# Kernel tuning notes

Measured on AMD Instinct MI355X. Metric: run time of the kernel, lower is better.

Reference implementation:

```python
import jax, jax.numpy as jnp
import numpy as np

H = 512          # hidden_size
SH = 120         # scoring_net_hidden_size
B = 1024         # batch
S = 64           # num_sentences


def setup_inputs() -> dict:
    key = jax.random.key(0)
    ks = jax.random.split(key, 12)
    sc = 0.05
    return {
        "C": jax.random.normal(ks[0], (B, S, H), jnp.float32),
        "Q": jax.random.normal(ks[1], (B, 1, H), jnp.float32),
        "prev_M": jax.random.normal(ks[2], (B, 1, H), jnp.float32),
        # scoring network params: fc1: 4H -> SH, fc2: SH -> 1
        "fc1_w": jax.random.normal(ks[3], (SH, 4 * H), jnp.float32) * sc,
        "fc1_b": jnp.zeros((SH,), jnp.float32),
        "fc2_w": jax.random.normal(ks[4], (1, SH), jnp.float32) * sc,
        "fc2_b": jnp.zeros((1,), jnp.float32),
        # GRU params (torch layout: rows ordered r, z, n)
        "W_ih": jax.random.normal(ks[5], (3 * H, H), jnp.float32) * sc,
        "W_hh": jax.random.normal(ks[6], (3 * H, H), jnp.float32) * sc,
        "b_ih": jnp.zeros((3 * H,), jnp.float32),
        "b_hh": jnp.zeros((3 * H,), jnp.float32),
    }


def reference(C, Q, prev_M, fc1_w, fc1_b, fc2_w, fc2_b, W_ih, W_hh, b_ih, b_hh):
    # --- scoring network (arch=1 feature vector) ---
    feat = jnp.concatenate(
        [C * Q, C * prev_M, jnp.abs(C - Q), jnp.abs(C - prev_M)], axis=2
    )  # [B, S, 4H]
    h1 = jnp.tanh(jnp.einsum("bsf,kf->bsk", feat, fc1_w) + fc1_b)
    G = jax.nn.sigmoid((jnp.einsum("bsk,ok->bso", h1, fc2_w) + fc2_b)[..., 0])  # [B, S]

    # --- gated GRU memory update over sentences ---
    xg_all = jnp.einsum("bsh,gh->bsg", C, W_ih) + b_ih  # [B, S, 3H] precomputed input gates

    def step(h, inp):
        xg, g = inp  # xg: [B, 3H], g: [B]
        hg = h @ W_hh.T + b_hh
        xr, xz, xn = jnp.split(xg, 3, axis=-1)
        hr, hz, hn = jnp.split(hg, 3, axis=-1)
        r = jax.nn.sigmoid(xr + hr)
        z = jax.nn.sigmoid(xz + hz)
        n = jnp.tanh(xn + r * hn)
        h_gru = (1.0 - z) * n + z * h          # standard torch GRU update
        g = g[:, None]
        h_new = g * h_gru + (1.0 - g) * h      # episodic gating
        return h_new, None

    h0 = jnp.zeros((C.shape[0], H), C.dtype)
    h_final, _ = jax.lax.scan(step, h0, (xg_all.transpose(1, 0, 2), G.T))
    return h_final[:, None, :]  # [B, 1, H]
```

## Files before the change

kernel.cpp:

```cpp
#include <hip/hip_runtime.h>
#include <hip/hip_bf16.h>

#define H_ 512
#define SH_ 120
#define B_ 1024
#define S_ 64

typedef __bf16 bf16x8 __attribute__((ext_vector_type(8)));
typedef float floatx4 __attribute__((ext_vector_type(4)));

__device__ __forceinline__ float bf2f(ushort u) {
    union { unsigned int i; float f; } v; v.i = ((unsigned int)u) << 16; return v.f;
}
__device__ __forceinline__ ushort f2bf(float f) {
    union { float f; unsigned int i; } v; v.f = f;
    unsigned int x = v.i;
    unsigned int r = (x + 0x7fffu + ((x >> 16) & 1u)) >> 16;
    return (ushort)r;
}

__device__ __attribute__((aligned(64))) unsigned g_prog[256];

__global__ __launch_bounds__(256) void prep_w(
    const float* __restrict__ fc1w, ushort* __restrict__ fc1wb,
    const float* __restrict__ Wih,  ushort* __restrict__ Wihb,
    const float* __restrict__ Whh,  ushort* __restrict__ Whhb)
{
    const int stride = gridDim.x * blockDim.x;
    const int tid = blockIdx.x * blockDim.x + threadIdx.x;
    for (int i = tid; i < 61440; i += stride) {
        const float4 v = ((const float4*)fc1w)[i];
        ushort4 o; o.x = f2bf(v.x); o.y = f2bf(v.y); o.z = f2bf(v.z); o.w = f2bf(v.w);
        ((ushort4*)fc1wb)[i] = o;
    }
    for (int i = tid; i < 196608; i += stride) {
        const float4 v = ((const float4*)Wih)[i];
        ushort4 o; o.x = f2bf(v.x); o.y = f2bf(v.y); o.z = f2bf(v.z); o.w = f2bf(v.w);
        ((ushort4*)Wihb)[i] = o;
    }
    for (int i = tid; i < 196608; i += stride) {
        const float4 v = ((const float4*)Whh)[i];
        ushort4 o; o.x = f2bf(v.x); o.y = f2bf(v.y); o.z = f2bf(v.z); o.w = f2bf(v.w);
        ((ushort4*)Whhb)[i] = o;
    }
}

__global__ __launch_bounds__(256) void g_kernel(
    const float* __restrict__ C, const float* __restrict__ Q,
    const float* __restrict__ M, const ushort* __restrict__ fc1wb,
    const float* __restrict__ fc1b, const float* __restrict__ fc2w,
    const float* __restrict__ fc2b, float* __restrict__ G)
{
    __shared__ float qrow[H_];
    __shared__ float mrow[H_];
    __shared__ __align__(16) ushort featT[64 * 72];
    __shared__ __align__(16) ushort wT[128 * 72];
    __shared__ float h1s[64 * 132];

    const int b = blockIdx.x;
    const int t = threadIdx.x;
    for (int i = t; i < H_; i += 256) { qrow[i] = Q[(size_t)b * H_ + i]; mrow[i] = M[(size_t)b * H_ + i]; }

    const int wrow = t >> 1;
    const int wc0  = (t & 1) * 32;
    if (wrow >= SH_) {
        uint4* dst = (uint4*)&wT[wrow * 72 + wc0];
        const uint4 z = {0u, 0u, 0u, 0u};
        dst[0] = z; dst[1] = z; dst[2] = z; dst[3] = z;
    }
    __syncthreads();

    const int lane = t & 63;
    const int wv   = t >> 6;
    const int quad = lane >> 4;
    const int l15  = lane & 15;
    const int arow = wv * 16 + l15;
    const int s    = t >> 2;
    const int c0   = (t & 3) * 16;

    floatx4 acc[8];
#pragma unroll
    for (int i = 0; i < 8; ++i) acc[i] = (floatx4){0.f, 0.f, 0.f, 0.f};

    for (int hc = 0; hc < H_; hc += 64) {
        float cr[16];
        {
            const float4* csrc = (const float4*)(C + ((size_t)b * S_ + s) * H_ + hc + c0);
            *(float4*)&cr[0]  = csrc[0];
            *(float4*)&cr[4]  = csrc[1];
            *(float4*)&cr[8]  = csrc[2];
            *(float4*)&cr[12] = csrc[3];
        }
#pragma unroll
        for (int seg = 0; seg < 4; ++seg) {
#pragma unroll
            for (int u = 0; u < 16; ++u) {
                const int kk = c0 + u;
                const float c = cr[u];
                const float o = (seg == 0 || seg == 2) ? qrow[hc + kk] : mrow[hc + kk];
                const float v = (seg < 2) ? c * o : fabsf(c - o);
                featT[s * 72 + kk] = f2bf(v);
            }
            if (wrow < SH_) {
                const uint4* src = (const uint4*)(fc1wb + (size_t)wrow * (4 * H_) + seg * H_ + hc + wc0);
                uint4* dst = (uint4*)&wT[wrow * 72 + wc0];
                dst[0] = src[0]; dst[1] = src[1]; dst[2] = src[2]; dst[3] = src[3];
            }
            __syncthreads();
#pragma unroll
            for (int ks = 0; ks < 64; ks += 32) {
                const int ao = ks + quad * 8;
                const bf16x8 af = *(const bf16x8*)&featT[arow * 72 + ao];
#pragma unroll
                for (int nt = 0; nt < 8; ++nt) {
                    const bf16x8 bfr = *(const bf16x8*)&wT[(nt * 16 + l15) * 72 + ao];
                    acc[nt] = __builtin_amdgcn_mfma_f32_16x16x32_bf16(af, bfr, acc[nt], 0, 0, 0);
                }
            }
            __syncthreads();
        }
    }

#pragma unroll
    for (int nt = 0; nt < 8; ++nt) {
        const int col = nt * 16 + l15;
        const float bias = (col < SH_) ? fc1b[col] : 0.f;
#pragma unroll
        for (int r = 0; r < 4; ++r) {
            const int row = wv * 16 + quad * 4 + r;
            h1s[row * 132 + col] = (col < SH_) ? tanhf(acc[nt][r] + bias) : 0.f;
        }
    }
    __syncthreads();
    {
        const int part = t & 3;
        float sum = 0.f;
        for (int k = part; k < SH_; k += 4) sum += h1s[s * 132 + k] * fc2w[k];
        sum += __shfl_xor(sum, 1);
        sum += __shfl_xor(sum, 2);
        if (part == 0) {
            const float logit = sum + fc2b[0];
            G[(size_t)b * S_ + s] = 1.f / (1.f + expf(-logit));
        }
    }
}

__global__ __launch_bounds__(256) void scan_all(
    const float* __restrict__ C, const ushort* __restrict__ Wihb,
    const ushort* __restrict__ Whhb, const float* __restrict__ bih,
    const float* __restrict__ bhh, const float* __restrict__ G,
    uint* __restrict__ hp0, uint* __restrict__ hp1,
    float* __restrict__ out)
{
    __shared__ __align__(16) ushort Whh_s[96 * 520];
    __shared__ __align__(16) char  smem_u[55296];
    ushort* AsU = (ushort*)smem_u;
    float*  gs  = (float*)smem_u;

    const int bx = blockIdx.x;
    const int jt = bx >> 4;
    const int bt = ((bx & 7) << 1) | ((bx >> 3) & 1);
    const int jb = jt * 32;
    const int bb = bt * 64;
    const int t  = threadIdx.x;
    const int lane = t & 63;
    const int wv   = t >> 6;
    const int quad = lane >> 4;
    const int l15  = lane & 15;
    const int mh   = wv >> 1;
    const int cset = wv & 1;
    const int crow = t >> 2;
    const int cc0  = (t & 3) * 16;
    const int hrow = t >> 2;
    const int hseg = t & 3;

    const unsigned vbase = __hip_atomic_load(&g_prog[(bt << 4) + jt],
                                             __ATOMIC_RELAXED, __HIP_MEMORY_SCOPE_AGENT);

#pragma unroll
    for (int i = 0; i < 24; ++i) {
        const int gid = i * 256 + t;
        const int row = gid >> 6;
        const int grp = gid & 63;
        const int grow = (row >> 5) * H_ + jb + (row & 31);
        *(uint4*)&Whh_s[row * 520 + grp * 8] =
            *(const uint4*)(Whhb + (size_t)grow * H_ + grp * 8);
    }

    float br_[2], bz_[2], bxn_[2], bhn_[2];
#pragma unroll
    for (int nt = 0; nt < 2; ++nt) {
        const int j = jb + nt * 16 + l15;
        br_[nt]  = bih[j] + bhh[j];
        bz_[nt]  = bih[H_ + j] + bhh[H_ + j];
        bxn_[nt] = bih[2 * H_ + j];
        bhn_[nt] = bhh[2 * H_ + j];
    }

    const int hold_kc  = (jb >> 6) << 6;
    const int hold_off = jb & 63;

    const uint* hr = hp0;
    uint*       hw = hp1;

    float cr[16];
    unsigned long long hreg[8];
    bf16x8 bi[3][2];

    auto load_c = [&](int tstep, int kc) {
        const float4* src = (const float4*)(C + ((size_t)(bb + crow) * S_ + tstep) * H_ + kc + cc0);
        *(float4*)&cr[0]  = src[0];
        *(float4*)&cr[4]  = src[1];
        *(float4*)&cr[8]  = src[2];
        *(float4*)&cr[12] = src[3];
    };
    auto load_h = [&](int kc) {
        const unsigned long long* src = (const unsigned long long*)
            (hr + (size_t)(bb + hrow) * H_ + kc + hseg * 16);
#pragma unroll
        for (int i = 0; i < 8; ++i)
            hreg[i] = __hip_atomic_load(src + i, __ATOMIC_RELAXED, __HIP_MEMORY_SCOPE_AGENT);
    };
    auto loadBi = [&](int kc) {
#pragma unroll
        for (int ct = 0; ct < 3; ++ct) {
            const int ctg = cset * 3 + ct;
            const size_t wrow = (size_t)((ctg >> 1) * H_ + jb + (ctg & 1) * 16 + l15) * H_;
#pragma unroll
            for (int ks2 = 0; ks2 < 2; ++ks2)
                bi[ct][ks2] = *(const bf16x8*)(Wihb + wrow + kc + ks2 * 32 + quad * 8);
        }
    };
    auto write_As = [&](int buf) {
        ushort* base = AsU + buf * 13824;
        __align__(16) ushort cb[16];
#pragma unroll
        for (int u = 0; u < 16; ++u) cb[u] = f2bf(cr[u]);
        uint4* d = (uint4*)&base[crow * 72 + cc0];
        d[0] = ((uint4*)cb)[0]; d[1] = ((uint4*)cb)[1];
        uint hiu[8], lou[8];
#pragma unroll
        for (int i = 0; i < 8; ++i) {
            const uint p0 = (uint)(hreg[i] & 0xFFFFFFFFull);
            const uint p1 = (uint)(hreg[i] >> 32);
            hiu[i] = (p0 >> 16) | (p1 & 0xFFFF0000u);
            lou[i] = (p0 & 0xFFFFu) | (p1 << 16);
        }
        uint4* dh = (uint4*)&base[4608 + hrow * 72 + hseg * 16];
        dh[0] = *(uint4*)&hiu[0]; dh[1] = *(uint4*)&hiu[4];
        uint4* dl = (uint4*)&base[9216 + hrow * 72 + hseg * 16];
        dl[0] = *(uint4*)&lou[0]; dl[1] = *(uint4*)&lou[4];
    };

    load_c(0, 0); loadBi(0); load_h(0);
    write_As(0);
    __syncthreads();

    for (int tstep = 0; tstep < S_; ++tstep) {
        float g_[4];
#pragma unroll
        for (int r4 = 0; r4 < 4; ++r4)
            g_[r4] = G[(size_t)(bb + wv * 16 + quad * 4 + r4) * S_ + tstep];

        floatx4 accA[2][3], accB[2][2];
#pragma unroll
        for (int rf = 0; rf < 2; ++rf) {
#pragma unroll
            for (int i = 0; i < 3; ++i) accA[rf][i] = (floatx4){0.f, 0.f, 0.f, 0.f};
#pragma unroll
            for (int i = 0; i < 2; ++i) accB[rf][i] = (floatx4){0.f, 0.f, 0.f, 0.f};
        }
        float hold_[2][4];

        for (int kc = 0; kc < H_; kc += 64) {
            const int cur = (kc >> 6) & 1;
            const int kn  = kc + 64;
            if (kn < H_) { load_c(tstep, kn); load_h(kn); }
            const ushort* Ac = AsU + cur * 13824;
            const ushort* Ah = Ac + 4608;
            const ushort* Al = Ac + 9216;
#pragma unroll
            for (int ks2 = 0; ks2 < 2; ++ks2) {
                const int ao = ks2 * 32 + quad * 8;
                bf16x8 a_c[2], a_hh[2], a_hl[2];
#pragma unroll
                for (int rf = 0; rf < 2; ++rf) {
                    const int ai = (mh * 32 + rf * 16 + l15) * 72 + ao;
                    a_c[rf]  = *(const bf16x8*)&Ac[ai];
                    a_hh[rf] = *(const bf16x8*)&Ah[ai];
                    a_hl[rf] = *(const bf16x8*)&Al[ai];
                }
#pragma unroll
                for (int ct = 0; ct < 3; ++ct) {
                    const int ctg = cset * 3 + ct;
                    const bf16x8 bh = *(const bf16x8*)
                        &Whh_s[((ctg >> 1) * 32 + (ctg & 1) * 16 + l15) * 520 + kc + ao];
#pragma unroll
                    for (int rf = 0; rf < 2; ++rf) {
                        if (ct >= 1 && cset == 1) {
                            accA[rf][ct]     = __builtin_amdgcn_mfma_f32_16x16x32_bf16(a_c[rf],  bi[ct][ks2], accA[rf][ct],     0, 0, 0);
                            accB[rf][ct - 1] = __builtin_amdgcn_mfma_f32_16x16x32_bf16(a_hh[rf], bh,          accB[rf][ct - 1], 0, 0, 0);
                            accB[rf][ct - 1] = __builtin_amdgcn_mfma_f32_16x16x32_bf16(a_hl[rf], bh,          accB[rf][ct - 1], 0, 0, 0);
                        } else {
                            accA[rf][ct] = __builtin_amdgcn_mfma_f32_16x16x32_bf16(a_c[rf],  bi[ct][ks2], accA[rf][ct], 0, 0, 0);
                            accA[rf][ct] = __builtin_amdgcn_mfma_f32_16x16x32_bf16(a_hh[rf], bh,          accA[rf][ct], 0, 0, 0);
                            accA[rf][ct] = __builtin_amdgcn_mfma_f32_16x16x32_bf16(a_hl[rf], bh,          accA[rf][ct], 0, 0, 0);
                        }
                    }
                }
            }
            if (kn < H_) { loadBi(kn); write_As(cur ^ 1); }
            if (kc == hold_kc) {
#pragma unroll
                for (int nt = 0; nt < 2; ++nt)
#pragma unroll
                    for (int r4 = 0; r4 < 4; ++r4) {
                        const int ai = (wv * 16 + quad * 4 + r4) * 72 + hold_off + nt * 16 + l15;
                        hold_[nt][r4] = bf2f(Ah[ai]) + bf2f(Al[ai]);
                    }
            }
            __syncthreads();
        }

#pragma unroll
        for (int rf = 0; rf < 2; ++rf)
#pragma unroll
        for (int ct = 0; ct < 3; ++ct) {
            const int ctg = cset * 3 + ct;
            const int go  = ctg >> 1;
            const int col = (ctg & 1) * 16 + l15;
            const int rbase = mh * 32 + rf * 16 + quad * 4;
#pragma unroll
            for (int r = 0; r < 4; ++r)
                gs[go * 2304 + (rbase + r) * 36 + col] = accA[rf][ct][r];
            if (ct >= 1 && cset == 1) {
#pragma unroll
                for (int r = 0; r < 4; ++r)
                    gs[3 * 2304 + (rbase + r) * 36 + col] = accB[rf][ct - 1][r];
            }
        }
        __syncthreads();

        const int last = (tstep == S_ - 1);
#pragma unroll
        for (int nt = 0; nt < 2; ++nt) {
            const int j = jb + nt * 16 + l15;
#pragma unroll
            for (int r4 = 0; r4 < 4; ++r4) {
                const int row = wv * 16 + quad * 4 + r4;
                const int b = bb + row;
                const size_t idx = (size_t)b * H_ + j;
                const int gidx = row * 36 + nt * 16 + l15;
                const float rrv = gs[0 * 2304 + gidx];
                const float zzv = gs[1 * 2304 + gidx];
                const float xnv = gs[2 * 2304 + gidx];
                const float hnv = gs[3 * 2304 + gidx];
                const float hold = hold_[nt][r4];
                const float g = g_[r4];
                const float rg = 1.f / (1.f + expf(-(rrv + br_[nt])));
                const float zg = 1.f / (1.f + expf(-(zzv + bz_[nt])));
                const float ng = tanhf(xnv + bxn_[nt] + rg * (hnv + bhn_[nt]));
                const float hgru = (1.f - zg) * ng + zg * hold;
                const float hnew = g * hgru + (1.f - g) * hold;
                const ushort hb = f2bf(hnew);
                const ushort hl = f2bf(hnew - bf2f(hb));
                __hip_atomic_store(&hw[idx], ((uint)hb << 16) | (uint)hl,
                                   __ATOMIC_RELAXED, __HIP_MEMORY_SCOPE_AGENT);
                if (last) out[idx] = hnew;
            }
        }
        if (last) break;

        { uint* tmp = hw; hw = (uint*)hr; hr = (const uint*)tmp; }

        load_c(tstep + 1, 0);
        loadBi(0);

        asm volatile("s_waitcnt vmcnt(0)" ::: "memory");
        __syncthreads();
        if (t == 0)
            __hip_atomic_store(&g_prog[(bt << 4) + jt], vbase + (unsigned)(tstep + 1),
                               __ATOMIC_RELAXED, __HIP_MEMORY_SCOPE_AGENT);
        if (wv == 0) {
            const unsigned tgt = vbase + (unsigned)(tstep + 1);
            const int slot = (bt << 4) + (t & 15);
            while (true) {
                const unsigned v = __hip_atomic_load(&g_prog[slot],
                                                     __ATOMIC_RELAXED, __HIP_MEMORY_SCOPE_AGENT);
                if (__all(v >= tgt)) break;
                __builtin_amdgcn_s_sleep(2);
            }
        }
        __syncthreads();

        load_h(0);
        write_As(0);
        __syncthreads();
    }
}

extern "C" void kernel_launch(void* const* d_in, const int* in_sizes, int n_in,
                              void* d_out, int out_size, void* d_ws, size_t ws_size,
                              hipStream_t stream) {
    (void)in_sizes; (void)n_in; (void)out_size; (void)ws_size;
    const float* C    = (const float*)d_in[0];
    const float* Q    = (const float*)d_in[1];
    const float* M    = (const float*)d_in[2];
    const float* fc1w = (const float*)d_in[3];
    const float* fc1b = (const float*)d_in[4];
    const float* fc2w = (const float*)d_in[5];
    const float* fc2b = (const float*)d_in[6];
    const float* Wih  = (const float*)d_in[7];
    const float* Whh  = (const float*)d_in[8];
    const float* bih  = (const float*)d_in[9];
    const float* bhh  = (const float*)d_in[10];
    float* out = (float*)d_out;

    char* ws = (char*)d_ws;
    float* Gbuf  = (float*)ws;
    uint*  hp0   = (uint*)(ws + 262144);
    uint*  hp1   = (uint*)(ws + 262144 + 2097152);
    ushort* fc1wb = (ushort*)(ws + 4456448);
    ushort* Wihb  = (ushort*)(ws + 4947968);
    ushort* Whhb  = (ushort*)(ws + 6520832);

    hipMemsetAsync(hp0, 0, 2097152, stream);

    prep_w<<<256, 256, 0, stream>>>(fc1w, fc1wb, Wih, Wihb, Whh, Whhb);
    g_kernel<<<B_, 256, 0, stream>>>(C, Q, M, fc1wb, fc1b, fc2w, fc2b, Gbuf);
    scan_all<<<256, 256, 0, stream>>>(C, Wihb, Whhb, bih, bhh, Gbuf,
                                      hp0, hp1, out);
}
```

Baseline: 1.541 ms.

## Double scan block threads and overlap input-gate GEMM with grid barrier wait

Scan kernel now uses 512 threads per block, so each wave covers 16 batch rows instead of 32. The C·W_ih input-gate product for the next step is computed straight from global memory into accumulators before the cross-block barrier spin, hiding that work behind the wait for other blocks. The recurrent loop only stages h hi/lo in LDS, and every wave now spins on the progress flags instead of wave 0 followed by a block sync. This trades more global loads of C and W_ih per wave, with no LDS staging for them, for more parallelism and latency hiding on the sequential path.

```diff
diff --git a/kernel.cpp b/kernel.cpp
--- a/kernel.cpp
+++ b/kernel.cpp
@@ -145,7 +145,7 @@
     }
 }
 
-__global__ __launch_bounds__(256) void scan_all(
+__global__ __launch_bounds__(512) void scan_all(
     const float* __restrict__ C, const ushort* __restrict__ Wihb,
     const ushort* __restrict__ Whhb, const float* __restrict__ bih,
     const float* __restrict__ bhh, const float* __restrict__ G,
@@ -153,9 +153,8 @@
     float* __restrict__ out)
 {
     __shared__ __align__(16) ushort Whh_s[96 * 520];
-    __shared__ __align__(16) char  smem_u[55296];
-    ushort* AsU = (ushort*)smem_u;
-    float*  gs  = (float*)smem_u;
+    __shared__ __align__(16) ushort AsU[4 * 4608];
+    float* gs = (float*)AsU;
 
     const int bx = blockIdx.x;
     const int jt = bx >> 4;
@@ -169,17 +168,13 @@
     const int l15  = lane & 15;
     const int mh   = wv >> 1;
     const int cset = wv & 1;
-    const int crow = t >> 2;
-    const int cc0  = (t & 3) * 16;
-    const int hrow = t >> 2;
-    const int hseg = t & 3;
 
     const unsigned vbase = __hip_atomic_load(&g_prog[(bt << 4) + jt],
                                              __ATOMIC_RELAXED, __HIP_MEMORY_SCOPE_AGENT);
 
 #pragma unroll
-    for (int i = 0; i < 24; ++i) {
-        const int gid = i * 256 + t;
+    for (int i = 0; i < 12; ++i) {
+        const int gid = i * 512 + t;
         const int row = gid >> 6;
         const int grp = gid & 63;
         const int grow = (row >> 5) * H_ + jb + (row & 31);
@@ -203,140 +198,147 @@
     const uint* hr = hp0;
     uint*       hw = hp1;
 
-    float cr[16];
-    unsigned long long hreg[8];
-    bf16x8 bi[3][2];
-
-    auto load_c = [&](int tstep, int kc) {
-        const float4* src = (const float4*)(C + ((size_t)(bb + crow) * S_ + tstep) * H_ + kc + cc0);
-        *(float4*)&cr[0]  = src[0];
-        *(float4*)&cr[4]  = src[1];
-        *(float4*)&cr[8]  = src[2];
-        *(float4*)&cr[12] = src[3];
-    };
+    unsigned long long hreg[4];
+
     auto load_h = [&](int kc) {
-        const unsigned long long* src = (const unsigned long long*)
-            (hr + (size_t)(bb + hrow) * H_ + kc + hseg * 16);
-#pragma unroll
-        for (int i = 0; i < 8; ++i)
-            hreg[i] = __hip_atomic_load(src + i, __ATOMIC_RELAXED, __HIP_MEMORY_SCOPE_AGENT);
-    };
-    auto loadBi = [&](int kc) {
-#pragma unroll
-        for (int ct = 0; ct < 3; ++ct) {
-            const int ctg = cset * 3 + ct;
-            const size_t wrow = (size_t)((ctg >> 1) * H_ + jb + (ctg & 1) * 16 + l15) * H_;
-#pragma unroll
-            for (int ks2 = 0; ks2 < 2; ++ks2)
-                bi[ct][ks2] = *(const bf16x8*)(Wihb + wrow + kc + ks2 * 32 + quad * 8);
+#pragma unroll
+        for (int i = 0; i < 2; ++i) {
+            const int chunk = i * 512 + t;
+            const int row = chunk >> 4;
+            const int c4  = (chunk & 15) * 4;
+            const unsigned long long* src = (const unsigned long long*)
+                (hr + (size_t)(bb + row) * H_ + kc + c4);
+            hreg[i * 2 + 0] = __hip_atomic_load(src,     __ATOMIC_RELAXED, __HIP_MEMORY_SCOPE_AGENT);
+            hreg[i * 2 + 1] = __hip_atomic_load(src + 1, __ATOMIC_RELAXED, __HIP_MEMORY_SCOPE_AGENT);
         }
     };
     auto write_As = [&](int buf) {
-        ushort* base = AsU + buf * 13824;
-        __align__(16) ushort cb[16];
-#pragma unroll
-        for (int u = 0; u < 16; ++u) cb[u] = f2bf(cr[u]);
-        uint4* d = (uint4*)&base[crow * 72 + cc0];
-        d[0] = ((uint4*)cb)[0]; d[1] = ((uint4*)cb)[1];
-        uint hiu[8], lou[8];
-#pragma unroll
-        for (int i = 0; i < 8; ++i) {
-            const uint p0 = (uint)(hreg[i] & 0xFFFFFFFFull);
-            const uint p1 = (uint)(hreg[i] >> 32);
-            hiu[i] = (p0 >> 16) | (p1 & 0xFFFF0000u);
-            lou[i] = (p0 & 0xFFFFu) | (p1 << 16);
-        }
-        uint4* dh = (uint4*)&base[4608 + hrow * 72 + hseg * 16];
-        dh[0] = *(uint4*)&hiu[0]; dh[1] = *(uint4*)&hiu[4];
-        uint4* dl = (uint4*)&base[9216 + hrow * 72 + hseg * 16];
-        dl[0] = *(uint4*)&lou[0]; dl[1] = *(uint4*)&lou[4];
+        ushort* hi_p = AsU + (buf * 2 + 0) * 4608;
+        ushort* lo_p = AsU + (buf * 2 + 1) * 4608;
+#pragma unroll
+        for (int i = 0; i < 2; ++i) {
+            const int chunk = i * 512 + t;
+            const int row = chunk >> 4;
+            const int c4  = (chunk & 15) * 4;
+            const uint p0 = (uint)hreg[2 * i],     p1 = (uint)(hreg[2 * i] >> 32);
+            const uint p2 = (uint)hreg[2 * i + 1], p3 = (uint)(hreg[2 * i + 1] >> 32);
+            uint2 hi2, lo2;
+            hi2.x = (p0 >> 16) | (p1 & 0xFFFF0000u);
+            hi2.y = (p2 >> 16) | (p3 & 0xFFFF0000u);
+            lo2.x = (p0 & 0xFFFFu) | (p1 << 16);
+            lo2.y = (p2 & 0xFFFFu) | (p3 << 16);
+            *(uint2*)&hi_p[row * 72 + c4] = hi2;
+            *(uint2*)&lo_p[row * 72 + c4] = lo2;
+        }
     };
 
-    load_c(0, 0); loadBi(0); load_h(0);
+    floatx4 accA[3], accB[2];
+    auto zero_acc = [&]() {
+#pragma unroll
+        for (int i = 0; i < 3; ++i) accA[i] = (floatx4){0.f, 0.f, 0.f, 0.f};
+#pragma unroll
+        for (int i = 0; i < 2; ++i) accB[i] = (floatx4){0.f, 0.f, 0.f, 0.f};
+    };
+
+    auto phaseB = [&](int tstep) {
+        const float* crow = C + ((size_t)(bb + mh * 16 + l15) * S_ + tstep) * H_;
+#pragma unroll 2
+        for (int kc = 0; kc < H_; kc += 64) {
+            bf16x8 bi0[3], bi1[3];
+#pragma unroll
+            for (int ct = 0; ct < 3; ++ct) {
+                const int ctg = cset * 3 + ct;
+                const ushort* wr = Wihb +
+                    (size_t)((ctg >> 1) * H_ + jb + (ctg & 1) * 16 + l15) * H_ + kc + quad * 8;
+                bi0[ct] = *(const bf16x8*)wr;
+                bi1[ct] = *(const bf16x8*)(wr + 32);
+            }
+            float cf[16];
+            *(float4*)&cf[0]  = *(const float4*)(crow + kc + quad * 8);
+            *(float4*)&cf[4]  = *(const float4*)(crow + kc + quad * 8 + 4);
+            *(float4*)&cf[8]  = *(const float4*)(crow + kc + 32 + quad * 8);
+            *(float4*)&cf[12] = *(const float4*)(crow + kc + 32 + quad * 8 + 4);
+            __align__(16) ushort cb[16];
+#pragma unroll
+            for (int u = 0; u < 16; ++u) cb[u] = f2bf(cf[u]);
+            const bf16x8 ac0 = *(const bf16x8*)&cb[0];
+            const bf16x8 ac1 = *(const bf16x8*)&cb[8];
+#pragma unroll
+            for (int ct = 0; ct < 3; ++ct)
+                accA[ct] = __builtin_amdgcn_mfma_f32_16x16x32_bf16(ac0, bi0[ct], accA[ct], 0, 0, 0);
+#pragma unroll
+            for (int ct = 0; ct < 3; ++ct)
+                accA[ct] = __builtin_amdgcn_mfma_f32_16x16x32_bf16(ac1, bi1[ct], accA[ct], 0, 0, 0);
+        }
+    };
+
+    zero_acc();
+    phaseB(0);
+    load_h(0);
     write_As(0);
     __syncthreads();
 
+#pragma unroll 1
     for (int tstep = 0; tstep < S_; ++tstep) {
-        float g_[4];
-#pragma unroll
-        for (int r4 = 0; r4 < 4; ++r4)
-            g_[r4] = G[(size_t)(bb + wv * 16 + quad * 4 + r4) * S_ + tstep];
-
-        floatx4 accA[2][3], accB[2][2];
-#pragma unroll
-        for (int rf = 0; rf < 2; ++rf) {
-#pragma unroll
-            for (int i = 0; i < 3; ++i) accA[rf][i] = (floatx4){0.f, 0.f, 0.f, 0.f};
-#pragma unroll
-            for (int i = 0; i < 2; ++i) accB[rf][i] = (floatx4){0.f, 0.f, 0.f, 0.f};
-        }
-        float hold_[2][4];
+        float g_[2];
+#pragma unroll
+        for (int r2 = 0; r2 < 2; ++r2)
+            g_[r2] = G[(size_t)(bb + wv * 8 + quad * 2 + r2) * S_ + tstep];
+
+        float hold_[2][2];
 
         for (int kc = 0; kc < H_; kc += 64) {
             const int cur = (kc >> 6) & 1;
             const int kn  = kc + 64;
-            if (kn < H_) { load_c(tstep, kn); load_h(kn); }
-            const ushort* Ac = AsU + cur * 13824;
-            const ushort* Ah = Ac + 4608;
-            const ushort* Al = Ac + 9216;
+            if (kn < H_) load_h(kn);
+            const ushort* Ah = AsU + (cur * 2 + 0) * 4608;
+            const ushort* Al = AsU + (cur * 2 + 1) * 4608;
 #pragma unroll
             for (int ks2 = 0; ks2 < 2; ++ks2) {
                 const int ao = ks2 * 32 + quad * 8;
-                bf16x8 a_c[2], a_hh[2], a_hl[2];
-#pragma unroll
-                for (int rf = 0; rf < 2; ++rf) {
-                    const int ai = (mh * 32 + rf * 16 + l15) * 72 + ao;
-                    a_c[rf]  = *(const bf16x8*)&Ac[ai];
-                    a_hh[rf] = *(const bf16x8*)&Ah[ai];
-                    a_hl[rf] = *(const bf16x8*)&Al[ai];
-                }
+                const int ai = (mh * 16 + l15) * 72 + ao;
+                const bf16x8 a_hh = *(const bf16x8*)&Ah[ai];
+                const bf16x8 a_hl = *(const bf16x8*)&Al[ai];
 #pragma unroll
                 for (int ct = 0; ct < 3; ++ct) {
                     const int ctg = cset * 3 + ct;
                     const bf16x8 bh = *(const bf16x8*)
                         &Whh_s[((ctg >> 1) * 32 + (ctg & 1) * 16 + l15) * 520 + kc + ao];
-#pragma unroll
-                    for (int rf = 0; rf < 2; ++rf) {
-                        if (ct >= 1 && cset == 1) {
-                            accA[rf][ct]     = __builtin_amdgcn_mfma_f32_16x16x32_bf16(a_c[rf],  bi[ct][ks2], accA[rf][ct],     0, 0, 0);
-                            accB[rf][ct - 1] = __builtin_amdgcn_mfma_f32_16x16x32_bf16(a_hh[rf], bh,          accB[rf][ct - 1], 0, 0, 0);
-                            accB[rf][ct - 1] = __builtin_amdgcn_mfma_f32_16x16x32_bf16(a_hl[rf], bh,          accB[rf][ct - 1], 0, 0, 0);
-                        } else {
-                            accA[rf][ct] = __builtin_amdgcn_mfma_f32_16x16x32_bf16(a_c[rf],  bi[ct][ks2], accA[rf][ct], 0, 0, 0);
-                            accA[rf][ct] = __builtin_amdgcn_mfma_f32_16x16x32_bf16(a_hh[rf], bh,          accA[rf][ct], 0, 0, 0);
-                            accA[rf][ct] = __builtin_amdgcn_mfma_f32_16x16x32_bf16(a_hl[rf], bh,          accA[rf][ct], 0, 0, 0);
-                        }
+                    if (cset == 1 && ct >= 1) {
+                        accB[ct - 1] = __builtin_amdgcn_mfma_f32_16x16x32_bf16(a_hh, bh, accB[ct - 1], 0, 0, 0);
+                        accB[ct - 1] = __builtin_amdgcn_mfma_f32_16x16x32_bf16(a_hl, bh, accB[ct - 1], 0, 0, 0);
+                    } else {
+                        accA[ct] = __builtin_amdgcn_mfma_f32_16x16x32_bf16(a_hh, bh, accA[ct], 0, 0, 0);
+                        accA[ct] = __builtin_amdgcn_mfma_f32_16x16x32_bf16(a_hl, bh, accA[ct], 0, 0, 0);
                     }
                 }
             }
-            if (kn < H_) { loadBi(kn); write_As(cur ^ 1); }
             if (kc == hold_kc) {
 #pragma unroll
                 for (int nt = 0; nt < 2; ++nt)
 #pragma unroll
-                    for (int r4 = 0; r4 < 4; ++r4) {
-                        const int ai = (wv * 16 + quad * 4 + r4) * 72 + hold_off + nt * 16 + l15;
-                        hold_[nt][r4] = bf2f(Ah[ai]) + bf2f(Al[ai]);
+                    for (int r2 = 0; r2 < 2; ++r2) {
+                        const int ai = (wv * 8 + quad * 2 + r2) * 72 + hold_off + nt * 16 + l15;
+                        hold_[nt][r2] = bf2f(Ah[ai]) + bf2f(Al[ai]);
                     }
             }
+            if (kn < H_) write_As(cur ^ 1);
             __syncthreads();
         }
 
-#pragma unroll
-        for (int rf = 0; rf < 2; ++rf)
 #pragma unroll
         for (int ct = 0; ct < 3; ++ct) {
             const int ctg = cset * 3 + ct;
             const int go  = ctg >> 1;
             const int col = (ctg & 1) * 16 + l15;
-            const int rbase = mh * 32 + rf * 16 + quad * 4;
+            const int rbase = mh * 16 + quad * 4;
 #pragma unroll
             for (int r = 0; r < 4; ++r)
-                gs[go * 2304 + (rbase + r) * 36 + col] = accA[rf][ct][r];
-            if (ct >= 1 && cset == 1) {
+                gs[go * 2304 + (rbase + r) * 36 + col] = accA[ct][r];
+            if (cset == 1 && ct >= 1) {
 #pragma unroll
                 for (int r = 0; r < 4; ++r)
-                    gs[3 * 2304 + (rbase + r) * 36 + col] = accB[rf][ct - 1][r];
+                    gs[3 * 2304 + (rbase + r) * 36 + col] = accB[ct - 1][r];
             }
         }
         __syncthreads();
@@ -346,17 +348,16 @@
         for (int nt = 0; nt < 2; ++nt) {
             const int j = jb + nt * 16 + l15;
 #pragma unroll
-            for (int r4 = 0; r4 < 4; ++r4) {
-                const int row = wv * 16 + quad * 4 + r4;
-                const int b = bb + row;
-                const size_t idx = (size_t)b * H_ + j;
+            for (int r2 = 0; r2 < 2; ++r2) {
+                const int row = wv * 8 + quad * 2 + r2;
+                const size_t idx = (size_t)(bb + row) * H_ + j;
                 const int gidx = row * 36 + nt * 16 + l15;
                 const float rrv = gs[0 * 2304 + gidx];
                 const float zzv = gs[1 * 2304 + gidx];
                 const float xnv = gs[2 * 2304 + gidx];
                 const float hnv = gs[3 * 2304 + gidx];
-                const float hold = hold_[nt][r4];
-                const float g = g_[r4];
+                const float hold = hold_[nt][r2];
+                const float g = g_[r2];
                 const float rg = 1.f / (1.f + expf(-(rrv + br_[nt])));
                 const float zg = 1.f / (1.f + expf(-(zzv + bz_[nt])));
                 const float ng = tanhf(xnv + bxn_[nt] + rg * (hnv + bhn_[nt]));
@@ -371,28 +372,26 @@
         }
         if (last) break;
 
-        { uint* tmp = hw; hw = (uint*)hr; hr = (const uint*)tmp; }
-
-        load_c(tstep + 1, 0);
-        loadBi(0);
-
         asm volatile("s_waitcnt vmcnt(0)" ::: "memory");
         __syncthreads();
         if (t == 0)
             __hip_atomic_store(&g_prog[(bt << 4) + jt], vbase + (unsigned)(tstep + 1),
                                __ATOMIC_RELAXED, __HIP_MEMORY_SCOPE_AGENT);
-        if (wv == 0) {
+        { uint* tmp = hw; hw = (uint*)hr; hr = (const uint*)tmp; }
+
+        zero_acc();
+        phaseB(tstep + 1);
+
+        {
             const unsigned tgt = vbase + (unsigned)(tstep + 1);
-            const int slot = (bt << 4) + (t & 15);
+            const int slot = (bt << 4) + (lane & 15);
             while (true) {
                 const unsigned v = __hip_atomic_load(&g_prog[slot],
                                                      __ATOMIC_RELAXED, __HIP_MEMORY_SCOPE_AGENT);
                 if (__all(v >= tgt)) break;
-                __builtin_amdgcn_s_sleep(2);
-            }
-        }
-        __syncthreads();
-
+                __builtin_amdgcn_s_sleep(1);
+            }
+        }
         load_h(0);
         write_As(0);
         __syncthreads();
@@ -428,6 +427,6 @@
 
     prep_w<<<256, 256, 0, stream>>>(fc1w, fc1wb, Wih, Wihb, Whh, Whhb);
     g_kernel<<<B_, 256, 0, stream>>>(C, Q, M, fc1wb, fc1b, fc2w, fc2b, Gbuf);
-    scan_all<<<256, 256, 0, stream>>>(C, Wihb, Whhb, bih, bhh, Gbuf,
+    scan_all<<<256, 512, 0, stream>>>(C, Wihb, Whhb, bih, bhh, Gbuf,
                                       hp0, hp1, out);
 }
```

Result: slower. 1.881 ms (+22.1%).
